# Kernel optimization log

Hardware: AMD Instinct MI355X
Metric: run time of the kernel (lower is better)

The kernel has to match this reference:

```python
import jax, jax.numpy as jnp
import numpy as np

N_VARS = 100_000
N_CLAUSES = 420_000
NNZ = 3 * N_CLAUSES
N_GRAPHS = 32
FM = 64
QM = 64
ROUNDS = 8
EPS = 1e-6


def _dense_init(key, din, dout):
    lim = float(np.sqrt(6.0 / (din + dout)))
    W = jax.random.uniform(key, (din, dout), jnp.float32, -lim, lim)
    return W, jnp.zeros((dout,), jnp.float32)


def setup_inputs() -> dict:
    key = jax.random.key(0)
    ks = jax.random.split(key, 16)
    # sparse literal-clause incidence: 3 literals per clause (3-SAT)
    lit_idx = jax.random.randint(ks[0], (NNZ,), 0, 2 * N_VARS)
    clause_idx = jnp.repeat(jnp.arange(N_CLAUSES), 3)
    # graph membership (batched formulas), contiguous per graph
    var_gid = jnp.sort(jax.random.randint(ks[1], (N_VARS,), 0, N_GRAPHS))
    clause_gid = jnp.sort(jax.random.randint(ks[2], (N_CLAUSES,), 0, N_GRAPHS))
    inp = {"lit_idx": lit_idx, "clause_idx": clause_idx,
           "var_gid": var_gid, "clause_gid": clause_gid}
    dims = {
        "vq": [(FM + 4, QM), (QM, QM)],                       # variables_query
        "cm": [(2 * FM, 2 * FM), (2 * FM, FM + QM)],          # clause_update
        "ug": [(4 * FM, 2 * FM), (2 * FM, 2 * FM), (2 * FM, FM)],  # update_gate
        "co": [(FM, FM), (FM, 1)],                             # clauses_mask_output
    }
    i = 3
    for name, layers in dims.items():
        for l, (din, dout) in enumerate(layers):
            W, b = _dense_init(ks[i], din, dout)
            i += 1
            inp[f"{name}_W{l}"] = W
            inp[f"{name}_b{l}"] = b
    return inp


def _mlp(x, params):
    for W, b in params[:-1]:
        x = jax.nn.relu(x @ W + b)
    W, b = params[-1]
    return x @ W + b


def _pair_norm(x, gid, n_graphs):
    # per-graph mean-subtract + RMS normalize (PairNorm, subtract_mean=True)
    cnt = jnp.maximum(
        jax.ops.segment_sum(jnp.ones((x.shape[0],), x.dtype), gid, num_segments=n_graphs), 1.0)[:, None]
    mean = jax.ops.segment_sum(x, gid, num_segments=n_graphs) / cnt
    x = x - mean[gid]
    var = jax.ops.segment_sum(jnp.mean(x * x, axis=-1, keepdims=True), gid, num_segments=n_graphs) / cnt
    return x * jax.lax.rsqrt(var[gid] + EPS)


def _forward(lit_idx, clause_idx, var_gid, clause_gid,
             vq_W0, vq_b0, vq_W1, vq_b1,
             cm_W0, cm_b0, cm_W1, cm_b1,
             ug_W0, ug_b0, ug_W1, ug_b1, ug_W2, ug_b2,
             co_W0, co_b0, co_W1, co_b1):
    vq = [(vq_W0, vq_b0), (vq_W1, vq_b1)]
    cm = [(cm_W0, cm_b0), (cm_W1, cm_b1)]
    ug = [(ug_W0, ug_b0), (ug_W1, ug_b1), (ug_W2, ug_b2)]
    co = [(co_W0, co_b0), (co_W1, co_b1)]
    V = var_gid.shape[0]
    C = clause_gid.shape[0]
    L = 2 * V  # literals

    variables = jnp.ones((V, FM), jnp.float32)
    clauses = jnp.ones((C, FM), jnp.float32)

    ones_e = jnp.ones((lit_idx.shape[0],), jnp.float32)
    lit_degree = jax.ops.segment_sum(ones_e, lit_idx, num_segments=L)[:, None]  # [2V,1]
    degree_weight = jax.lax.rsqrt(jnp.maximum(lit_degree, 1.0))
    var_degree_weight = 4.0 * jax.lax.rsqrt(jnp.maximum(lit_degree[:V] + lit_degree[V:], 1.0))

    def clause_loss(q):
        # softplus_loss_adj: exp(-(adj^T @ softplus([q; -q])))
        lits = jax.nn.softplus(jnp.concatenate([q, -q], axis=0))  # [2V, QM]
        cv = jax.ops.segment_sum(lits[lit_idx], clause_idx, num_segments=C)  # [C, QM]
        cl = jnp.exp(-cv)
        return jnp.sum(cl), cl

    def body(carry, key):
        variables, clauses = carry
        v1 = jnp.concatenate(
            [variables, jax.random.normal(key, (V, 4), jnp.float32)], axis=-1)
        query = _mlp(v1, vq)  # [V, QM]
        (_, clauses_loss), q_grad = jax.value_and_grad(clause_loss, has_aux=True)(query)
        variables_grad = q_grad * var_degree_weight

        clause_unit = jnp.concatenate([clauses, 4.0 * clauses_loss], axis=-1)  # [C, 2*FM]
        clause_data = _mlp(clause_unit, cm)  # [C, FM+QM]
        variables_loss_all = clause_data[:, :QM]
        new_clause = _pair_norm(clause_data[:, QM:], clause_gid, N_GRAPHS) * 0.25
        clauses = new_clause + 0.1 * clauses

        # adj @ variables_loss_all : scatter clause features to literals
        variables_loss = jax.ops.segment_sum(
            variables_loss_all[clause_idx], lit_idx, num_segments=L) * degree_weight  # [2V, QM]
        unit = jnp.concatenate(
            [variables_grad, variables, variables_loss[:V], variables_loss[V:]], axis=-1)
        new_variables = _pair_norm(_mlp(unit, ug), var_gid, N_GRAPHS) * 0.25
        variables = new_variables + 0.1 * variables

        logits = _mlp(clauses, co)  # [C, 1]
        variables = jax.lax.stop_gradient(variables) * 0.2 + variables * 0.8
        clauses = jax.lax.stop_gradient(clauses) * 0.2  # + clauses * 0.0
        return (variables, clauses), logits

    keys = jax.random.split(jax.random.key(42), ROUNDS + 1)
    (_, _), logits_seq = jax.lax.scan(body, (variables, clauses), keys[:ROUNDS])
    last_logits = logits_seq[-1]
    noise = jax.random.normal(keys[ROUNDS], last_logits.shape, jnp.float32)
    return jnp.squeeze(jax.nn.sigmoid(last_logits + noise), axis=-1)  # [C]


def reference(lit_idx, clause_idx, var_gid, clause_gid,
              vq_W0, vq_b0, vq_W1, vq_b1,
              cm_W0, cm_b0, cm_W1, cm_b1,
              ug_W0, ug_b0, ug_W1, ug_b1, ug_W2, ug_b2,
              co_W0, co_b0, co_W1, co_b1):
    return _forward(lit_idx, clause_idx, var_gid, clause_gid,
                    vq_W0, vq_b0, vq_W1, vq_b1,
                    cm_W0, cm_b0, cm_W1, cm_b1,
                    ug_W0, ug_b0, ug_W1, ug_b1, ug_W2, ug_b2,
                    co_W0, co_b0, co_W1, co_b1)
```

## Files before the change

### kernel.cpp

```cpp
#include <hip/hip_runtime.h>
#include <hip/hip_bf16.h>
#include <cstdint>
#include <cstddef>

constexpr int V_N = 100000;
constexpr int C_N = 420000;
constexpr int L_N = 2 * V_N;
constexpr int E_N = 3 * C_N;
constexpr int NGR = 32;
constexpr int NROUNDS = 8;

using bf16 = __hip_bfloat16;
typedef __attribute__((ext_vector_type(8))) short short8;
typedef __attribute__((ext_vector_type(4))) float float4v;

__device__ inline float b2f(bf16 h) { return __bfloat162float(h); }
__device__ inline bf16 f2b(float f) { return __float2bfloat16(f); }
__device__ inline float sb2f(short s) { return __uint_as_float(((uint32_t)(uint16_t)s) << 16); }
__device__ inline short f2sb(float f) { bf16 h = f2b(f); return *(short*)&h; }

template<typename T> __device__ inline float loadT(const T* p);
template<> __device__ inline float loadT<float>(const float* p) { return *p; }
template<> __device__ inline float loadT<bf16>(const bf16* p) { return b2f(*p); }

template<typename TX> __device__ inline void load8(const TX* p, float* v);
template<> __device__ inline void load8<bf16>(const bf16* p, float* v) {
  short8 s = *(const short8*)p;
#pragma unroll
  for (int e = 0; e < 8; e++) v[e] = sb2f(s[e]);
}
template<> __device__ inline void load8<float>(const float* p, float* v) {
  float4 a = *(const float4*)p;
  float4 b = *(const float4*)(p + 4);
  v[0] = a.x; v[1] = a.y; v[2] = a.z; v[3] = a.w;
  v[4] = b.x; v[5] = b.y; v[6] = b.z; v[7] = b.w;
}

__device__ inline float wload(const void* W, size_t idx, int isf32) {
  return isf32 ? ((const float*)W)[idx] : b2f(((const bf16*)W)[idx]);
}

__host__ __device__ inline void tf2x32(uint32_t k0, uint32_t k1,
                                       uint32_t x0, uint32_t x1,
                                       uint32_t* o0, uint32_t* o1) {
  uint32_t ks2 = k0 ^ k1 ^ 0x1BD11BDAu;
  x0 += k0; x1 += k1;
#define TFR(d) do { x0 += x1; x1 = (x1 << (d)) | (x1 >> (32 - (d))); x1 ^= x0; } while (0)
  TFR(13); TFR(15); TFR(26); TFR(6);
  x0 += k1;  x1 += ks2 + 1u;
  TFR(17); TFR(29); TFR(16); TFR(24);
  x0 += ks2; x1 += k0 + 2u;
  TFR(13); TFR(15); TFR(26); TFR(6);
  x0 += k0;  x1 += k1 + 3u;
  TFR(17); TFR(29); TFR(16); TFR(24);
  x0 += k1;  x1 += ks2 + 4u;
  TFR(13); TFR(15); TFR(26); TFR(6);
  x0 += ks2; x1 += k0 + 5u;
#undef TFR
  *o0 = x0; *o1 = x1;
}

__device__ inline uint32_t part_bits(uint32_t ka, uint32_t kb, uint32_t e) {
  uint32_t h1, h2;
  tf2x32(ka, kb, 0u, e, &h1, &h2);
  return h1 ^ h2;
}

__device__ inline float erfinv_f32(float x) {
  float w = -log1pf(-x * x);
  float p;
  if (w < 5.0f) {
    w -= 2.5f;
    p = 2.81022636e-08f;
    p = fmaf(p, w, 3.43273939e-07f);
    p = fmaf(p, w, -3.5233877e-06f);
    p = fmaf(p, w, -4.39150654e-06f);
    p = fmaf(p, w, 0.00021858087f);
    p = fmaf(p, w, -0.00125372503f);
    p = fmaf(p, w, -0.00417768164f);
    p = fmaf(p, w, 0.246640727f);
    p = fmaf(p, w, 1.50140941f);
  } else {
    w = sqrtf(w) - 3.0f;
    p = -0.000200214257f;
    p = fmaf(p, w, 0.000100950558f);
    p = fmaf(p, w, 0.00134934322f);
    p = fmaf(p, w, -0.00367342844f);
    p = fmaf(p, w, 0.00573950773f);
    p = fmaf(p, w, -0.0076224613f);
    p = fmaf(p, w, 0.00943887047f);
    p = fmaf(p, w, 1.00167406f);
    p = fmaf(p, w, 2.83297682f);
  }
  return p * x;
}

__device__ inline float normal_from_bits(uint32_t bits) {
  float u01 = __uint_as_float((bits >> 9) | 0x3f800000u) - 1.0f;
  const float lo = -0.99999994f;
  float u = u01 * 2.0f + lo;
  u = fmaxf(lo, u);
  return 1.41421356f * erfinv_f32(u);
}

__device__ inline float softplusf(float x) {
  return (x > 0.0f) ? x + log1pf(expf(-x)) : log1pf(expf(x));
}

__global__ void fill_f32(float* p, size_t n, float v) {
  size_t i = (size_t)blockIdx.x * blockDim.x + threadIdx.x;
  size_t stride = (size_t)gridDim.x * blockDim.x;
  for (; i < n; i += stride) p[i] = v;
}
__global__ void fill_u32(uint32_t* p, size_t n, uint32_t v) {
  size_t i = (size_t)blockIdx.x * blockDim.x + threadIdx.x;
  size_t stride = (size_t)gridDim.x * blockDim.x;
  for (; i < n; i += stride) p[i] = v;
}
__global__ void fill_b16(bf16* p, size_t n, float v) {
  size_t i = (size_t)blockIdx.x * blockDim.x + threadIdx.x;
  size_t stride = (size_t)gridDim.x * blockDim.x;
  bf16 b = f2b(v);
  for (; i < n; i += stride) p[i] = b;
}

__global__ void detect_dtype_kernel(const uint32_t* __restrict__ w, int* __restrict__ flag) {
  if (blockIdx.x == 0 && threadIdx.x == 0) {
    int votes = 0;
    for (int i = 0; i < 16; i++) {
      uint32_t lo = w[i] & 0xFFFFu;
      uint32_t e = (lo >> 7) & 0xFFu;
      if (e >= 0x70u && e < 0x80u) votes++;
    }
    *flag = (votes >= 12) ? 0 : 1;
  }
}

__global__ void pack_w_kernel(const void* __restrict__ W, const int* __restrict__ flagp,
                              int realK, int Kpad, int M, int Wld, int wcol0,
                              int srow0, float sscale, bf16* __restrict__ out) {
  int idx = blockIdx.x * 256 + threadIdx.x;
  if (idx >= Kpad * M) return;
  int j = idx & 7;
  int lane = (idx >> 3) & 63;
  int t = idx >> 9;
  int MT = M / 16;
  int kt = t / MT, nt = t - kt * MT;
  int k = kt * 32 + (lane >> 4) * 8 + j;
  int n = nt * 16 + (lane & 15);
  float v = 0.0f;
  if (k < realK) {
    v = wload(W, (size_t)k * Wld + wcol0 + n, *flagp);
    if (k >= srow0) v *= sscale;
  }
  out[idx] = f2b(v);
}

__global__ void count_deg_kernel(const int* __restrict__ lit, int* __restrict__ deg) {
  int e = blockIdx.x * 256 + threadIdx.x;
  if (e < E_N) atomicAdd(&deg[lit[e]], 1);
}

__global__ void hist32_kernel(const int* __restrict__ gid, int n, int* __restrict__ out) {
  __shared__ int bins[NGR];
  int t = threadIdx.x;
  if (t < NGR) bins[t] = 0;
  __syncthreads();
  int i = blockIdx.x * 256 + t;
  if (i < n) atomicAdd(&bins[gid[i]], 1);
  __syncthreads();
  if (t < NGR && bins[t] > 0) atomicAdd(&out[t], bins[t]);
}

__global__ void weights_kernel(const int* __restrict__ deg,
                               float* __restrict__ dw, float* __restrict__ vdw) {
  int l = blockIdx.x * 256 + threadIdx.x;
  if (l < L_N) dw[l] = rsqrtf(fmaxf((float)deg[l], 1.0f));
  if (l < V_N) vdw[l] = 4.0f * rsqrtf(fmaxf((float)(deg[l] + deg[l + V_N]), 1.0f));
}

__global__ void scan_kernel(const int* __restrict__ deg, int* __restrict__ offs) {
  __shared__ int part[256];
  __shared__ int base[257];
  int t = threadIdx.x;
  const int CH = (L_N + 255) / 256;
  int i0 = t * CH, i1 = min(L_N, i0 + CH);
  int s = 0;
  for (int i = i0; i < i1; i++) s += deg[i];
  part[t] = s;
  __syncthreads();
  if (t == 0) {
    int acc = 0;
    for (int j = 0; j < 256; j++) { base[j] = acc; acc += part[j]; }
    base[256] = acc;
  }
  __syncthreads();
  int acc = base[t];
  for (int i = i0; i < i1; i++) { offs[i] = acc; acc += deg[i]; }
  if (t == 255) offs[L_N] = base[256];
}

__global__ void csr_fill_kernel(const int* __restrict__ lit,
                                const int* __restrict__ offs, int* __restrict__ cursor,
                                int* __restrict__ csr) {
  int e = blockIdx.x * 256 + threadIdx.x;
  if (e < E_N) {
    int l = lit[e];
    int p = atomicAdd(&cursor[l], 1);
    csr[offs[l] + p] = e / 3;
  }
}

__global__ void noise4_kernel(bf16* __restrict__ Zb, uint32_t ka, uint32_t kb) {
  int idx = blockIdx.x * 256 + threadIdx.x;
  if (idx >= V_N * 4) return;
  int v = idx >> 2, j = idx & 3;
  Zb[(size_t)v * 32 + j] = f2b(normal_from_bits(part_bits(ka, kb, (uint32_t)idx)));
}


__global__ __launch_bounds__(256) void vq_fused_kernel(
    const bf16* __restrict__ variables, const bf16* __restrict__ Zb,
    const bf16* __restrict__ W0p, const void* __restrict__ b0,
    const bf16* __restrict__ W1p, const void* __restrict__ b1,
    const int* __restrict__ flagp, bf16* __restrict__ Q,
    bf16* __restrict__ SP, int N) {
  __shared__ bf16 hs[64][72];
  int tid = threadIdx.x;
  int wave = tid >> 6, lane = tid & 63, quad = lane >> 4, m16 = lane & 15;
  int row = blockIdx.x * 64 + wave * 16 + m16;
  int rowc = min(row, N - 1);
  int isf32 = *flagp;
  float4v acc[4];
#pragma unroll
  for (int nt = 0; nt < 4; nt++) acc[nt] = (float4v){0.f, 0.f, 0.f, 0.f};
  const short8* w0 = (const short8*)W0p;
  for (int k0 = 0; k0 < 96; k0 += 32) {
    int ks = k0 + quad * 8;
    const bf16* src = (ks < 64) ? variables + (size_t)rowc * 64 + ks
                                : Zb + (size_t)rowc * 32 + (ks - 64);
    short8 a = *(const short8*)src;
#pragma unroll
    for (int nt = 0; nt < 4; nt++) {
      short8 b = w0[((k0 >> 5) * 4 + nt) * 64 + lane];
      acc[nt] = __builtin_amdgcn_mfma_f32_16x16x32_bf16(a, b, acc[nt], 0, 0, 0);
    }
  }
  int rl = wave * 16 + quad * 4;
#pragma unroll
  for (int nt = 0; nt < 4; nt++) {
    int col = nt * 16 + m16;
    float bv = wload(b0, col, isf32);
#pragma unroll
    for (int i = 0; i < 4; i++)
      hs[rl + i][col] = f2b(fmaxf(acc[nt][i] + bv, 0.0f));
  }
  __syncthreads();
  float4v acc2[4];
#pragma unroll
  for (int nt = 0; nt < 4; nt++) acc2[nt] = (float4v){0.f, 0.f, 0.f, 0.f};
  const short8* w1 = (const short8*)W1p;
  for (int k0 = 0; k0 < 64; k0 += 32) {
    short8 a = *(const short8*)&hs[wave * 16 + m16][k0 + quad * 8];
#pragma unroll
    for (int nt = 0; nt < 4; nt++) {
      short8 b = w1[((k0 >> 5) * 4 + nt) * 64 + lane];
      acc2[nt] = __builtin_amdgcn_mfma_f32_16x16x32_bf16(a, b, acc2[nt], 0, 0, 0);
    }
  }
  int rbase = blockIdx.x * 64 + wave * 16 + quad * 4;
#pragma unroll
  for (int nt = 0; nt < 4; nt++) {
    int col = nt * 16 + m16;
    float bv = wload(b1, col, isf32);
#pragma unroll
    for (int i = 0; i < 4; i++) {
      int r = rbase + i;
      if (r < N) {
        float q = acc2[nt][i] + bv;
        Q[(size_t)r * 64 + col] = f2b(q);
        SP[(size_t)r * 64 + col] = f2b(softplusf(q));
        SP[(size_t)(r + V_N) * 64 + col] = f2b(softplusf(-q));
      }
    }
  }
}

__global__ __launch_bounds__(256) void cm_fused_kernel(
    const bf16* __restrict__ clauses, const bf16* __restrict__ clb,
    const bf16* __restrict__ W0p, const void* __restrict__ b0,
    const bf16* __restrict__ W1p, const void* __restrict__ b1,
    const int* __restrict__ flagp,
    bf16* __restrict__ Dl, bf16* __restrict__ Dn, int N) {
  __shared__ bf16 hs[64][136];
  int tid = threadIdx.x;
  int wave = tid >> 6, lane = tid & 63, quad = lane >> 4, m16 = lane & 15;
  int row = blockIdx.x * 64 + wave * 16 + m16;
  int rowc = min(row, N - 1);
  int isf32 = *flagp;
  float4v acc[8];
#pragma unroll
  for (int nt = 0; nt < 8; nt++) acc[nt] = (float4v){0.f, 0.f, 0.f, 0.f};
  const short8* w0 = (const short8*)W0p;
  for (int k0 = 0; k0 < 128; k0 += 32) {
    int ks = k0 + quad * 8;
    const bf16* src = (ks < 64) ? clauses + (size_t)rowc * 64 + ks
                                : clb + (size_t)rowc * 64 + (ks - 64);
    short8 a = *(const short8*)src;
#pragma unroll
    for (int nt = 0; nt < 8; nt++) {
      short8 b = w0[((k0 >> 5) * 8 + nt) * 64 + lane];
      acc[nt] = __builtin_amdgcn_mfma_f32_16x16x32_bf16(a, b, acc[nt], 0, 0, 0);
    }
  }
  int rl = wave * 16 + quad * 4;
#pragma unroll
  for (int nt = 0; nt < 8; nt++) {
    int col = nt * 16 + m16;
    float bv = wload(b0, col, isf32);
#pragma unroll
    for (int i = 0; i < 4; i++)
      hs[rl + i][col] = f2b(fmaxf(acc[nt][i] + bv, 0.0f));
  }
  __syncthreads();
#pragma unroll
  for (int nt = 0; nt < 8; nt++) acc[nt] = (float4v){0.f, 0.f, 0.f, 0.f};
  const short8* w1 = (const short8*)W1p;
  for (int k0 = 0; k0 < 128; k0 += 32) {
    short8 a = *(const short8*)&hs[wave * 16 + m16][k0 + quad * 8];
#pragma unroll
    for (int nt = 0; nt < 8; nt++) {
      short8 b = w1[((k0 >> 5) * 8 + nt) * 64 + lane];
      acc[nt] = __builtin_amdgcn_mfma_f32_16x16x32_bf16(a, b, acc[nt], 0, 0, 0);
    }
  }
  int rbase = blockIdx.x * 64 + wave * 16 + quad * 4;
#pragma unroll
  for (int nt = 0; nt < 8; nt++) {
    int col = nt * 16 + m16;
    float bv = wload(b1, col, isf32);
#pragma unroll
    for (int i = 0; i < 4; i++) {
      int r = rbase + i;
      if (r < N) {
        float v = acc[nt][i] + bv;
        if (col < 64) Dl[(size_t)r * 64 + col] = f2b(v);
        else          Dn[(size_t)r * 64 + (col - 64)] = f2b(v);
      }
    }
  }
}

__global__ __launch_bounds__(256) void ug_fused_kernel(
    const bf16* __restrict__ QG, const bf16* __restrict__ variables,
    const bf16* __restrict__ VLb,
    const bf16* __restrict__ W0p, const void* __restrict__ b0,
    const bf16* __restrict__ W1p, const void* __restrict__ b1,
    const bf16* __restrict__ W2p, const void* __restrict__ b2,
    const int* __restrict__ flagp, float* __restrict__ NV, int N) {
  __shared__ bf16 h1[64][136];
  __shared__ bf16 h2[64][136];
  int tid = threadIdx.x;
  int wave = tid >> 6, lane = tid & 63, quad = lane >> 4, m16 = lane & 15;
  int row = blockIdx.x * 64 + wave * 16 + m16;
  int rowc = min(row, N - 1);
  int isf32 = *flagp;
  int rl = wave * 16 + quad * 4;
  float4v acc[8];
#pragma unroll
  for (int nt = 0; nt < 8; nt++) acc[nt] = (float4v){0.f, 0.f, 0.f, 0.f};
  const short8* w0 = (const short8*)W0p;
  for (int k0 = 0; k0 < 256; k0 += 32) {
    int ks = k0 + quad * 8;
    const bf16* src;
    if (ks < 64)       src = QG + (size_t)rowc * 64 + ks;
    else if (ks < 128) src = variables + (size_t)rowc * 64 + (ks - 64);
    else               src = VLb + (size_t)rowc * 128 + (ks - 128);
    short8 a = *(const short8*)src;
#pragma unroll
    for (int nt = 0; nt < 8; nt++) {
      short8 b = w0[((k0 >> 5) * 8 + nt) * 64 + lane];
      acc[nt] = __builtin_amdgcn_mfma_f32_16x16x32_bf16(a, b, acc[nt], 0, 0, 0);
    }
  }
#pragma unroll
  for (int nt = 0; nt < 8; nt++) {
    int col = nt * 16 + m16;
    float bv = wload(b0, col, isf32);
#pragma unroll
    for (int i = 0; i < 4; i++)
      h1[rl + i][col] = f2b(fmaxf(acc[nt][i] + bv, 0.0f));
  }
  __syncthreads();
#pragma unroll
  for (int nt = 0; nt < 8; nt++) acc[nt] = (float4v){0.f, 0.f, 0.f, 0.f};
  const short8* w1 = (const short8*)W1p;
  for (int k0 = 0; k0 < 128; k0 += 32) {
    short8 a = *(const short8*)&h1[wave * 16 + m16][k0 + quad * 8];
#pragma unroll
    for (int nt = 0; nt < 8; nt++) {
      short8 b = w1[((k0 >> 5) * 8 + nt) * 64 + lane];
      acc[nt] = __builtin_amdgcn_mfma_f32_16x16x32_bf16(a, b, acc[nt], 0, 0, 0);
    }
  }
#pragma unroll
  for (int nt = 0; nt < 8; nt++) {
    int col = nt * 16 + m16;
    float bv = wload(b1, col, isf32);
#pragma unroll
    for (int i = 0; i < 4; i++)
      h2[rl + i][col] = f2b(fmaxf(acc[nt][i] + bv, 0.0f));
  }
  __syncthreads();
  float4v acc3[4];
#pragma unroll
  for (int nt = 0; nt < 4; nt++) acc3[nt] = (float4v){0.f, 0.f, 0.f, 0.f};
  const short8* w2 = (const short8*)W2p;
  for (int k0 = 0; k0 < 128; k0 += 32) {
    short8 a = *(const short8*)&h2[wave * 16 + m16][k0 + quad * 8];
#pragma unroll
    for (int nt = 0; nt < 4; nt++) {
      short8 b = w2[((k0 >> 5) * 4 + nt) * 64 + lane];
      acc3[nt] = __builtin_amdgcn_mfma_f32_16x16x32_bf16(a, b, acc3[nt], 0, 0, 0);
    }
  }
  int rbase = blockIdx.x * 64 + wave * 16 + quad * 4;
#pragma unroll
  for (int nt = 0; nt < 4; nt++) {
    int col = nt * 16 + m16;
    float bv = wload(b2, col, isf32);
#pragma unroll
    for (int i = 0; i < 4; i++) {
      int r = rbase + i;
      if (r < N) NV[(size_t)r * 64 + col] = acc3[nt][i] + bv;
    }
  }
}

__global__ void cl_kernel(const bf16* __restrict__ SP, const int* __restrict__ lit,
                          bf16* __restrict__ cl, float* __restrict__ stats) {
  if (blockIdx.x == 0) {
    for (int i = threadIdx.x; i < 4096; i += 256) stats[i] = 0.0f;
  }
  int t = blockIdx.x * 256 + threadIdx.x;
  int c = t >> 3, j = t & 7;
  if (c >= C_N) return;
  int l0 = lit[3 * c], l1 = lit[3 * c + 1], l2 = lit[3 * c + 2];
  short8 s0 = *(const short8*)&SP[(size_t)l0 * 64 + j * 8];
  short8 s1 = *(const short8*)&SP[(size_t)l1 * 64 + j * 8];
  short8 s2 = *(const short8*)&SP[(size_t)l2 * 64 + j * 8];
  short8 r;
#pragma unroll
  for (int e = 0; e < 8; e++) {
    float cv = sb2f(s0[e]) + sb2f(s1[e]) + sb2f(s2[e]);
    r[e] = f2sb(expf(-cv));
  }
  *(short8*)&cl[(size_t)c * 64 + j * 8] = r;
}

__global__ void qgrad_kernel(const bf16* __restrict__ Q, const bf16* __restrict__ clb,
                             const int* __restrict__ csr, const int* __restrict__ offs,
                             const float* __restrict__ vdw, bf16* __restrict__ QG) {
  int t = blockIdx.x * 256 + threadIdx.x;
  int v = t >> 3, j = t & 7;
  if (v >= V_N) return;
  float gp[8], gn[8];
#pragma unroll
  for (int e = 0; e < 8; e++) { gp[e] = 0.0f; gn[e] = 0.0f; }
  int p0 = offs[v], p1 = offs[v + 1];
  for (int p = p0; p < p1; p++) {
    short8 x = *(const short8*)&clb[(size_t)csr[p] * 64 + j * 8];
#pragma unroll
    for (int e = 0; e < 8; e++) gp[e] += sb2f(x[e]);
  }
  p0 = offs[v + V_N]; p1 = offs[v + V_N + 1];
  for (int p = p0; p < p1; p++) {
    short8 x = *(const short8*)&clb[(size_t)csr[p] * 64 + j * 8];
#pragma unroll
    for (int e = 0; e < 8; e++) gn[e] += sb2f(x[e]);
  }
  short8 qv = *(const short8*)&Q[(size_t)v * 64 + j * 8];
  float w = vdw[v];
  short8 r;
#pragma unroll
  for (int e = 0; e < 8; e++) {
    float q = sb2f(qv[e]);
    float sp = 1.0f / (1.0f + expf(-q));
    float sn = 1.0f / (1.0f + expf(q));
    r[e] = f2sb((-sp * gp[e] + sn * gn[e]) * w);
  }
  *(short8*)&QG[(size_t)v * 64 + j * 8] = r;
}

__global__ void vlb_gather_kernel(const bf16* __restrict__ Dl, const int* __restrict__ csr,
                                  const int* __restrict__ offs, const float* __restrict__ dw,
                                  bf16* __restrict__ VLb, float* __restrict__ stats) {
  if (blockIdx.x == 0) {
    for (int i = threadIdx.x; i < 4096; i += 256) stats[i] = 0.0f;
  }
  int t = blockIdx.x * 256 + threadIdx.x;
  int l = t >> 3, j = t & 7;
  if (l >= L_N) return;
  float s[8];
#pragma unroll
  for (int e = 0; e < 8; e++) s[e] = 0.0f;
  int p0 = offs[l], p1 = offs[l + 1];
  for (int p = p0; p < p1; p++) {
    short8 x = *(const short8*)&Dl[(size_t)csr[p] * 64 + j * 8];
#pragma unroll
    for (int e = 0; e < 8; e++) s[e] += sb2f(x[e]);
  }
  float w = dw[l];
  size_t v = (l < V_N) ? (size_t)l : (size_t)(l - V_N);
  int col = (l < V_N) ? 0 : 64;
  short8 r;
#pragma unroll
  for (int e = 0; e < 8; e++) r[e] = f2sb(s[e] * w);
  *(short8*)&VLb[v * 128 + col + j * 8] = r;
}

template<typename TX>
__global__ void pn_stats_kernel(const TX* __restrict__ X,
                                const int* __restrict__ gid, int n,
                                float* __restrict__ S1, float* __restrict__ S2) {
  int wave = blockIdx.x * blockDim.y + threadIdx.y;
  int nw = gridDim.x * blockDim.y;
  int chunk = (n + nw - 1) / nw;
  int i0 = wave * chunk;
  if (i0 >= n) return;
  int i1 = min(n, i0 + chunk);
  int lane = threadIdx.x;
  int sub = lane >> 3, j = lane & 7;
  float a1[8], a2[8];
#pragma unroll
  for (int e = 0; e < 8; e++) { a1[e] = 0.0f; a2[e] = 0.0f; }
  int ifirst = i0 + sub;
  if (ifirst >= i1) return;
  int g = gid[ifirst];
  for (int i = ifirst; i < i1; i += 8) {
    int gi = gid[i];
    if (gi != g) {
#pragma unroll
      for (int e = 0; e < 8; e++) {
        atomicAdd(&S1[g * 64 + j * 8 + e], a1[e]);
        atomicAdd(&S2[g * 64 + j * 8 + e], a2[e]);
        a1[e] = 0.0f; a2[e] = 0.0f;
      }
      g = gi;
    }
    float x[8];
    load8(&X[(size_t)i * 64 + j * 8], x);
#pragma unroll
    for (int e = 0; e < 8; e++) { a1[e] += x[e]; a2[e] += x[e] * x[e]; }
  }
#pragma unroll
  for (int e = 0; e < 8; e++) {
    atomicAdd(&S1[g * 64 + j * 8 + e], a1[e]);
    atomicAdd(&S2[g * 64 + j * 8 + e], a2[e]);
  }
}

template<typename TX>
__global__ void pn_apply_kernel(const TX* __restrict__ X,
                                const int* __restrict__ gid, int n,
                                const int* __restrict__ cnt, const float* __restrict__ S1,
                                const float* __restrict__ S2, bf16* __restrict__ state,
                                float post) {
  int t = blockIdx.x * 256 + threadIdx.x;
  int i = t >> 3, j = t & 7;
  if (i >= n) return;
  int g = gid[i];
  float c = fmaxf((float)cnt[g], 1.0f);
  float m[8], tv = 0.0f;
#pragma unroll
  for (int e = 0; e < 8; e++) {
    m[e] = S1[g * 64 + j * 8 + e] / c;
    tv += S2[g * 64 + j * 8 + e] / c - m[e] * m[e];
  }
#pragma unroll
  for (int o = 1; o < 8; o <<= 1) tv += __shfl_xor(tv, o);
  float var = fmaxf(tv, 0.0f) * (1.0f / 64.0f);
  float rs = rsqrtf(var + 1e-6f);
  float x[8];
  load8(&X[(size_t)i * 64 + j * 8], x);
  short8 st = *(const short8*)&state[(size_t)i * 64 + j * 8];
  short8 r;
#pragma unroll
  for (int e = 0; e < 8; e++) {
    float xn = (x[e] - m[e]) * rs;
    r[e] = f2sb((xn * 0.25f + 0.1f * sb2f(st[e])) * post);
  }
  *(short8*)&state[(size_t)i * 64 + j * 8] = r;
}

__global__ __launch_bounds__(256) void co_final_kernel(
    const bf16* __restrict__ clauses, const bf16* __restrict__ W0p,
    const void* __restrict__ b0, const void* __restrict__ W1,
    const void* __restrict__ b1, const int* __restrict__ flagp,
    uint32_t ka, uint32_t kb, float* __restrict__ out) {
  int tid = threadIdx.x;
  int wave = tid >> 6, lane = tid & 63, quad = lane >> 4, m16 = lane & 15;
  int row = blockIdx.x * 64 + wave * 16 + m16;
  int rowc = min(row, C_N - 1);
  int isf32 = *flagp;
  float4v acc[4];
#pragma unroll
  for (int nt = 0; nt < 4; nt++) acc[nt] = (float4v){0.f, 0.f, 0.f, 0.f};
  const short8* w0 = (const short8*)W0p;
  for (int k0 = 0; k0 < 64; k0 += 32) {
    short8 a = *(const short8*)&clauses[(size_t)rowc * 64 + k0 + quad * 8];
#pragma unroll
    for (int nt = 0; nt < 4; nt++) {
      short8 b = w0[((k0 >> 5) * 4 + nt) * 64 + lane];
      acc[nt] = __builtin_amdgcn_mfma_f32_16x16x32_bf16(a, b, acc[nt], 0, 0, 0);
    }
  }
  float s[4] = {0.f, 0.f, 0.f, 0.f};
#pragma unroll
  for (int nt = 0; nt < 4; nt++) {
    int col = nt * 16 + m16;
    float bv = wload(b0, col, isf32);
    float w1v = wload(W1, col, isf32);
#pragma unroll
    for (int i = 0; i < 4; i++) s[i] += fmaxf(acc[nt][i] + bv, 0.0f) * w1v;
  }
#pragma unroll
  for (int o = 1; o < 16; o <<= 1) {
#pragma unroll
    for (int i = 0; i < 4; i++) s[i] += __shfl_xor(s[i], o);
  }
  if (m16 == 0) {
    int rbase = blockIdx.x * 64 + wave * 16 + quad * 4;
    float bb = wload(b1, 0, isf32);
#pragma unroll
    for (int i = 0; i < 4; i++) {
      int r = rbase + i;
      if (r < C_N) {
        float lg = s[i] + bb + normal_from_bits(part_bits(ka, kb, (uint32_t)r));
        out[r] = 1.0f / (1.0f + expf(-lg));
      }
    }
  }
}

extern "C" void kernel_launch(void* const* d_in, const int* in_sizes, int n_in,
                              void* d_out, int out_size, void* d_ws, size_t ws_size,
                              hipStream_t stream) {
  (void)in_sizes; (void)n_in; (void)out_size;
  const int* lit_idx    = (const int*)d_in[0];
  const int* var_gid    = (const int*)d_in[2];
  const int* clause_gid = (const int*)d_in[3];
  const void* vq_W0 = d_in[4];
  const void* vq_b0 = d_in[5];
  const void* vq_W1 = d_in[6];
  const void* vq_b1 = d_in[7];
  const void* cm_W0 = d_in[8];
  const void* cm_b0 = d_in[9];
  const void* cm_W1 = d_in[10];
  const void* cm_b1 = d_in[11];
  const void* ug_W0 = d_in[12];
  const void* ug_b0 = d_in[13];
  const void* ug_W1 = d_in[14];
  const void* ug_b1 = d_in[15];
  const void* ug_W2 = d_in[16];
  const void* ug_b2 = d_in[17];
  const void* co_W0 = d_in[18];
  const void* co_b0 = d_in[19];
  const void* co_W1 = d_in[20];
  const void* co_b1 = d_in[21];
  float* out = (float*)d_out;

  char* ws = (char*)d_ws;
  size_t off = 0;
  auto alloc = [&](size_t bytes) -> void* {
    void* p = ws + off;
    off = (off + bytes + 255) & ~(size_t)255;
    return p;
  };
  bf16* variables = (bf16*)alloc((size_t)V_N * 64 * 2);
  bf16* clauses   = (bf16*)alloc((size_t)C_N * 64 * 2);
  char* ZE        = (char*)alloc((size_t)C_N * 64 * 2);
  char* ZD        = (char*)alloc((size_t)C_N * 64 * 2);
  bf16* QG        = (bf16*)alloc((size_t)V_N * 64 * 2);
  bf16* Q         = (bf16*)alloc((size_t)V_N * 64 * 2);
  bf16* Zb        = (bf16*)alloc((size_t)V_N * 32 * 2);
  int*  izone     = (int*)alloc((size_t)(2 * L_N + 64) * 4);
  int*  offs      = (int*)alloc((size_t)(L_N + 1) * 4);
  int*  csr       = (int*)alloc((size_t)E_N * 4);
  float* deg_f    = (float*)alloc((size_t)L_N * 4);
  float* vdw      = (float*)alloc((size_t)V_N * 4);
  float* stats    = (float*)alloc((size_t)4096 * 4);
  int*   wflag    = (int*)alloc(256);
  bf16* vq_W0p = (bf16*)alloc((size_t)96 * 64 * 2);
  bf16* vq_W1p = (bf16*)alloc((size_t)64 * 64 * 2);
  bf16* cm_W0p = (bf16*)alloc((size_t)128 * 128 * 2);
  bf16* cm_W1p = (bf16*)alloc((size_t)128 * 128 * 2);
  bf16* ug_W0p = (bf16*)alloc((size_t)256 * 128 * 2);
  bf16* ug_W1p = (bf16*)alloc((size_t)128 * 128 * 2);
  bf16* ug_W2p = (bf16*)alloc((size_t)128 * 64 * 2);
  bf16* co_W0p = (bf16*)alloc((size_t)64 * 64 * 2);
  size_t need = off;

  auto nb = [](int n, int per) { return (n + per - 1) / per; };

  if (ws_size < need) {
    fill_f32<<<nb(C_N, 256), 256, 0, stream>>>(out, (size_t)C_N, 0.5f);
    return;
  }

  bf16* clb = (bf16*)ZE;
  bf16* Dn  = (bf16*)ZE;
  bf16* VLb = (bf16*)ZE;
  bf16* SP  = (bf16*)ZD;
  bf16* Dl  = (bf16*)ZD;
  float* NV = (float*)ZD;

  int* deg_i  = izone;
  int* cursor = izone + L_N;
  int* cntv   = izone + 2 * L_N;
  int* cntc   = cntv + 32;
  float* S1 = stats;
  float* S2 = stats + 2048;

  uint32_t kw0[9], kw1[9];
  for (int i = 0; i < 9; i++) tf2x32(0u, 42u, 0u, (uint32_t)i, &kw0[i], &kw1[i]);

  dim3 wb(64, 4);
  const int BIG = 1 << 30;

  detect_dtype_kernel<<<1, 64, 0, stream>>>((const uint32_t*)vq_W0, wflag);
  fill_u32<<<nb(2 * L_N + 64, 256), 256, 0, stream>>>((uint32_t*)izone, (size_t)(2 * L_N + 64), 0u);
  count_deg_kernel<<<nb(E_N, 256), 256, 0, stream>>>(lit_idx, deg_i);
  hist32_kernel<<<nb(V_N, 256), 256, 0, stream>>>(var_gid, V_N, cntv);
  hist32_kernel<<<nb(C_N, 256), 256, 0, stream>>>(clause_gid, C_N, cntc);
  weights_kernel<<<nb(L_N, 256), 256, 0, stream>>>(deg_i, deg_f, vdw);
  scan_kernel<<<1, 256, 0, stream>>>(deg_i, offs);
  csr_fill_kernel<<<nb(E_N, 256), 256, 0, stream>>>(lit_idx, offs, cursor, csr);
  fill_b16<<<2048, 256, 0, stream>>>(variables, (size_t)V_N * 64, 1.0f);
  fill_b16<<<2048, 256, 0, stream>>>(clauses, (size_t)C_N * 64, 1.0f);
  fill_b16<<<2048, 256, 0, stream>>>(Zb, (size_t)V_N * 32, 0.0f);
  pack_w_kernel<<<nb(96 * 64, 256), 256, 0, stream>>>(vq_W0, wflag, 68, 96, 64, 64, 0, BIG, 1.f, vq_W0p);
  pack_w_kernel<<<nb(64 * 64, 256), 256, 0, stream>>>(vq_W1, wflag, 64, 64, 64, 64, 0, BIG, 1.f, vq_W1p);
  pack_w_kernel<<<nb(128 * 128, 256), 256, 0, stream>>>(cm_W0, wflag, 128, 128, 128, 128, 0, 64, 4.f, cm_W0p);
  pack_w_kernel<<<nb(128 * 128, 256), 256, 0, stream>>>(cm_W1, wflag, 128, 128, 128, 128, 0, BIG, 1.f, cm_W1p);
  pack_w_kernel<<<nb(256 * 128, 256), 256, 0, stream>>>(ug_W0, wflag, 256, 256, 128, 128, 0, BIG, 1.f, ug_W0p);
  pack_w_kernel<<<nb(128 * 128, 256), 256, 0, stream>>>(ug_W1, wflag, 128, 128, 128, 128, 0, BIG, 1.f, ug_W1p);
  pack_w_kernel<<<nb(128 * 64, 256), 256, 0, stream>>>(ug_W2, wflag, 128, 128, 64, 64, 0, BIG, 1.f, ug_W2p);
  pack_w_kernel<<<nb(64 * 64, 256), 256, 0, stream>>>(co_W0, wflag, 64, 64, 64, 64, 0, BIG, 1.f, co_W0p);

  for (int r = 0; r < NROUNDS; r++) {
    noise4_kernel<<<nb(V_N * 4, 256), 256, 0, stream>>>(Zb, kw0[r], kw1[r]);
    vq_fused_kernel<<<nb(V_N, 64), 256, 0, stream>>>(
        variables, Zb, vq_W0p, vq_b0, vq_W1p, vq_b1, wflag, Q, SP, V_N);
    cl_kernel<<<nb(C_N * 8, 256), 256, 0, stream>>>(SP, lit_idx, clb, stats);
    qgrad_kernel<<<nb(V_N * 8, 256), 256, 0, stream>>>(Q, clb, csr, offs, vdw, QG);
    cm_fused_kernel<<<nb(C_N, 64), 256, 0, stream>>>(
        clauses, clb, cm_W0p, cm_b0, cm_W1p, cm_b1, wflag, Dl, Dn, C_N);
    pn_stats_kernel<bf16><<<128, wb, 0, stream>>>(Dn, clause_gid, C_N, S1, S2);
    pn_apply_kernel<bf16><<<nb(C_N * 8, 256), 256, 0, stream>>>(
        Dn, clause_gid, C_N, cntc, S1, S2, clauses, (r == NROUNDS - 1) ? 1.0f : 0.2f);
    vlb_gather_kernel<<<nb(L_N * 8, 256), 256, 0, stream>>>(Dl, csr, offs, deg_f, VLb, stats);
    ug_fused_kernel<<<nb(V_N, 64), 256, 0, stream>>>(
        QG, variables, VLb, ug_W0p, ug_b0, ug_W1p, ug_b1, ug_W2p, ug_b2,
        wflag, NV, V_N);
    pn_stats_kernel<float><<<128, wb, 0, stream>>>(NV, var_gid, V_N, S1, S2);
    pn_apply_kernel<float><<<nb(V_N * 8, 256), 256, 0, stream>>>(
        NV, var_gid, V_N, cntv, S1, S2, variables, 1.0f);
  }
  co_final_kernel<<<nb(C_N, 64), 256, 0, stream>>>(
      clauses, co_W0p, co_b0, co_W1, co_b1, wflag, kw0[8], kw1[8], out);
}
```

Baseline: 4.891 ms.

## Fuse noise generation into vq kernel and parallelize CSR offset scan

The per-round noise kernel and its Zb buffer are removed. The Gaussian noise for the four extra inputs is now generated inside vq_fused_kernel from the round key, and zero padding is built in registers. The single-block serial prefix scan over 200k literal degrees is replaced with a three-kernel block-parallel scan (partial sums, base scan, write). This removes one launch per round, the Zb memory traffic and a long serial setup kernel. In exchange it adds RNG arithmetic inside the vq kernel and two extra setup launches.

```diff
diff --git a/kernel.cpp b/kernel.cpp
--- a/kernel.cpp
+++ b/kernel.cpp
@@ -9,6 +9,7 @@
 constexpr int E_N = 3 * C_N;
 constexpr int NGR = 32;
 constexpr int NROUNDS = 8;
+constexpr int SCAN_NB = (L_N + 255) / 256;
 
 using bf16 = __hip_bfloat16;
 typedef __attribute__((ext_vector_type(8))) short short8;
@@ -179,25 +180,49 @@
   if (l < V_N) vdw[l] = 4.0f * rsqrtf(fmaxf((float)(deg[l] + deg[l + V_N]), 1.0f));
 }
 
-__global__ void scan_kernel(const int* __restrict__ deg, int* __restrict__ offs) {
-  __shared__ int part[256];
-  __shared__ int base[257];
+__global__ void scan_partial_kernel(const int* __restrict__ deg, int* __restrict__ part) {
+  __shared__ int red[256];
+  int b = blockIdx.x, t = threadIdx.x;
+  int i = b * 256 + t;
+  red[t] = (i < L_N) ? deg[i] : 0;
+  __syncthreads();
+  for (int o = 128; o > 0; o >>= 1) {
+    if (t < o) red[t] += red[t + o];
+    __syncthreads();
+  }
+  if (t == 0) part[b] = red[0];
+}
+
+__global__ void scan_base_kernel(const int* __restrict__ part, int* __restrict__ base) {
+  __shared__ int buf[SCAN_NB + 1];
   int t = threadIdx.x;
-  const int CH = (L_N + 255) / 256;
-  int i0 = t * CH, i1 = min(L_N, i0 + CH);
-  int s = 0;
-  for (int i = i0; i < i1; i++) s += deg[i];
-  part[t] = s;
+  for (int i = t; i < SCAN_NB; i += 256) buf[i] = part[i];
   __syncthreads();
   if (t == 0) {
     int acc = 0;
-    for (int j = 0; j < 256; j++) { base[j] = acc; acc += part[j]; }
-    base[256] = acc;
-  }
-  __syncthreads();
-  int acc = base[t];
-  for (int i = i0; i < i1; i++) { offs[i] = acc; acc += deg[i]; }
-  if (t == 255) offs[L_N] = base[256];
+    for (int i = 0; i < SCAN_NB; i++) { int v = buf[i]; buf[i] = acc; acc += v; }
+    buf[SCAN_NB] = acc;
+  }
+  __syncthreads();
+  for (int i = t; i <= SCAN_NB; i += 256) base[i] = buf[i];
+}
+
+__global__ void scan_write_kernel(const int* __restrict__ deg, const int* __restrict__ base,
+                                  int* __restrict__ offs) {
+  __shared__ int s[256];
+  int b = blockIdx.x, t = threadIdx.x;
+  int i = b * 256 + t;
+  int v = (i < L_N) ? deg[i] : 0;
+  s[t] = v;
+  __syncthreads();
+  for (int o = 1; o < 256; o <<= 1) {
+    int x = (t >= o) ? s[t - o] : 0;
+    __syncthreads();
+    s[t] += x;
+    __syncthreads();
+  }
+  if (i < L_N) offs[i] = base[b] + s[t] - v;
+  if (b == 0 && t == 0) offs[L_N] = base[SCAN_NB];
 }
 
 __global__ void csr_fill_kernel(const int* __restrict__ lit,
@@ -211,20 +236,13 @@
   }
 }
 
-__global__ void noise4_kernel(bf16* __restrict__ Zb, uint32_t ka, uint32_t kb) {
-  int idx = blockIdx.x * 256 + threadIdx.x;
-  if (idx >= V_N * 4) return;
-  int v = idx >> 2, j = idx & 3;
-  Zb[(size_t)v * 32 + j] = f2b(normal_from_bits(part_bits(ka, kb, (uint32_t)idx)));
-}
-
 
 __global__ __launch_bounds__(256) void vq_fused_kernel(
-    const bf16* __restrict__ variables, const bf16* __restrict__ Zb,
+    const bf16* __restrict__ variables,
     const bf16* __restrict__ W0p, const void* __restrict__ b0,
     const bf16* __restrict__ W1p, const void* __restrict__ b1,
-    const int* __restrict__ flagp, bf16* __restrict__ Q,
-    bf16* __restrict__ SP, int N) {
+    const int* __restrict__ flagp, uint32_t ka, uint32_t kb,
+    bf16* __restrict__ Q, bf16* __restrict__ SP, int N) {
   __shared__ bf16 hs[64][72];
   int tid = threadIdx.x;
   int wave = tid >> 6, lane = tid & 63, quad = lane >> 4, m16 = lane & 15;
@@ -237,9 +255,18 @@
   const short8* w0 = (const short8*)W0p;
   for (int k0 = 0; k0 < 96; k0 += 32) {
     int ks = k0 + quad * 8;
-    const bf16* src = (ks < 64) ? variables + (size_t)rowc * 64 + ks
-                                : Zb + (size_t)rowc * 32 + (ks - 64);
-    short8 a = *(const short8*)src;
+    short8 a;
+    if (ks < 64) {
+      a = *(const short8*)(variables + (size_t)rowc * 64 + ks);
+    } else if (ks == 64) {
+#pragma unroll
+      for (int e = 0; e < 8; e++)
+        a[e] = (e < 4)
+             ? f2sb(normal_from_bits(part_bits(ka, kb, (uint32_t)(rowc * 4 + e))))
+             : (short)0;
+    } else {
+      a = (short8){0, 0, 0, 0, 0, 0, 0, 0};
+    }
 #pragma unroll
     for (int nt = 0; nt < 4; nt++) {
       short8 b = w0[((k0 >> 5) * 4 + nt) * 64 + lane];
@@ -683,10 +710,10 @@
   char* ZD        = (char*)alloc((size_t)C_N * 64 * 2);
   bf16* QG        = (bf16*)alloc((size_t)V_N * 64 * 2);
   bf16* Q         = (bf16*)alloc((size_t)V_N * 64 * 2);
-  bf16* Zb        = (bf16*)alloc((size_t)V_N * 32 * 2);
   int*  izone     = (int*)alloc((size_t)(2 * L_N + 64) * 4);
   int*  offs      = (int*)alloc((size_t)(L_N + 1) * 4);
   int*  csr       = (int*)alloc((size_t)E_N * 4);
+  int*  spart     = (int*)alloc((size_t)(2 * SCAN_NB + 2) * 4);
   float* deg_f    = (float*)alloc((size_t)L_N * 4);
   float* vdw      = (float*)alloc((size_t)V_N * 4);
   float* stats    = (float*)alloc((size_t)4096 * 4);
@@ -719,6 +746,7 @@
   int* cursor = izone + L_N;
   int* cntv   = izone + 2 * L_N;
   int* cntc   = cntv + 32;
+  int* sbase  = spart + SCAN_NB;
   float* S1 = stats;
   float* S2 = stats + 2048;
 
@@ -734,11 +762,12 @@
   hist32_kernel<<<nb(V_N, 256), 256, 0, stream>>>(var_gid, V_N, cntv);
   hist32_kernel<<<nb(C_N, 256), 256, 0, stream>>>(clause_gid, C_N, cntc);
   weights_kernel<<<nb(L_N, 256), 256, 0, stream>>>(deg_i, deg_f, vdw);
-  scan_kernel<<<1, 256, 0, stream>>>(deg_i, offs);
+  scan_partial_kernel<<<SCAN_NB, 256, 0, stream>>>(deg_i, spart);
+  scan_base_kernel<<<1, 256, 0, stream>>>(spart, sbase);
+  scan_write_kernel<<<SCAN_NB, 256, 0, stream>>>(deg_i, sbase, offs);
   csr_fill_kernel<<<nb(E_N, 256), 256, 0, stream>>>(lit_idx, offs, cursor, csr);
   fill_b16<<<2048, 256, 0, stream>>>(variables, (size_t)V_N * 64, 1.0f);
   fill_b16<<<2048, 256, 0, stream>>>(clauses, (size_t)C_N * 64, 1.0f);
-  fill_b16<<<2048, 256, 0, stream>>>(Zb, (size_t)V_N * 32, 0.0f);
   pack_w_kernel<<<nb(96 * 64, 256), 256, 0, stream>>>(vq_W0, wflag, 68, 96, 64, 64, 0, BIG, 1.f, vq_W0p);
   pack_w_kernel<<<nb(64 * 64, 256), 256, 0, stream>>>(vq_W1, wflag, 64, 64, 64, 64, 0, BIG, 1.f, vq_W1p);
   pack_w_kernel<<<nb(128 * 128, 256), 256, 0, stream>>>(cm_W0, wflag, 128, 128, 128, 128, 0, 64, 4.f, cm_W0p);
@@ -749,9 +778,8 @@
   pack_w_kernel<<<nb(64 * 64, 256), 256, 0, stream>>>(co_W0, wflag, 64, 64, 64, 64, 0, BIG, 1.f, co_W0p);
 
   for (int r = 0; r < NROUNDS; r++) {
-    noise4_kernel<<<nb(V_N * 4, 256), 256, 0, stream>>>(Zb, kw0[r], kw1[r]);
     vq_fused_kernel<<<nb(V_N, 64), 256, 0, stream>>>(
-        variables, Zb, vq_W0p, vq_b0, vq_W1p, vq_b1, wflag, Q, SP, V_N);
+        variables, vq_W0p, vq_b0, vq_W1p, vq_b1, wflag, kw0[r], kw1[r], Q, SP, V_N);
     cl_kernel<<<nb(C_N * 8, 256), 256, 0, stream>>>(SP, lit_idx, clb, stats);
     qgrad_kernel<<<nb(V_N * 8, 256), 256, 0, stream>>>(Q, clb, csr, offs, vdw, QG);
     cm_fused_kernel<<<nb(C_N, 64), 256, 0, stream>>>(
```

After: 4.607 ms. 5.8% less time.
